# Optimization experiments

Measured on AMD Instinct MI355X. Metric: run time of the kernel, lower is better.

Reference implementation:

```python
import jax, jax.numpy as jnp
import numpy as np

B, N, C, H, F = 4, 256, 256, 8, 64  # batch, nodes, in_channels, heads, n_hidden


def setup_inputs() -> dict:
    key = jax.random.key(0)
    k1, k2, k3, k4, k5 = jax.random.split(key, 5)
    x = jax.random.normal(k1, (B, N, C), jnp.float32)
    W_l = jax.random.normal(k2, (C, H * F), jnp.float32) / np.sqrt(C)
    W_r = jax.random.normal(k3, (C, H * F), jnp.float32) / np.sqrt(C)
    attn_w = jax.random.normal(k4, (F,), jnp.float32) / np.sqrt(F)
    adj = jax.random.randint(k5, (N, N, H), 0, 2, jnp.int32)
    # guarantee at least one unmasked head per (i, j) pair so the
    # softmax-over-heads (dim=-1 in the source) never sees all -inf
    adj = adj.at[:, :, 0].set(1)
    return {"x": x, "W_l": W_l, "W_r": W_r, "attn_w": attn_w, "adj": adj}


def reference(x, W_l, W_r, attn_w, adj):
    b, n, _ = x.shape
    g_l = (x @ W_l).reshape(b, n, H, F)
    g_r = (x @ W_r).reshape(b, n, H, F)
    # torch: g_l.repeat(1,n,1,1) + g_r.repeat_interleave(n,dim=1), then
    # view(b,n,n,h,f)  =>  g_sum[b,i,j,h,f] = g_r[b,i] + g_l[b,j]
    g_sum = g_r[:, :, None] + g_l[:, None, :]          # [b,i,j,h,f]
    e = jnp.einsum('bijhf,f->bijh', jax.nn.leaky_relu(g_sum, 0.2), attn_w)
    e = jnp.where(adj == 0, -jnp.inf, e)               # adj broadcasts over batch
    a = jax.nn.softmax(e, axis=-1)                     # softmax over heads, per source (dim=-1)
    out = jnp.einsum('bijh,bjhf->bihf', a, g_r)        # aggregate over neighbors j
    return out.reshape(b, n, H * F)                    # is_concat=True
```

## Files before the change

### kernel.cpp

```cpp
#include <hip/hip_runtime.h>
#include <hip/hip_bf16.h>

typedef _Float16 h2 __attribute__((ext_vector_type(2)));

constexpr int kB = 4, kN = 256, kC = 256, kH = 8, kF = 64, kHF = 512;
constexpr int kIPB = 4;

union H2U { h2 h; unsigned int u; };

__global__ __launch_bounds__(256) void gat_gemm_kernel(
    const float* __restrict__ x,
    const float* __restrict__ Wl,
    const float* __restrict__ Wr,
    unsigned int* __restrict__ gl,
    unsigned int* __restrict__ gr)
{
    __shared__ float xs[4][kC];
    const int rowBase = blockIdx.x * 4;
    const float* Wm = (blockIdx.y == 0) ? Wl : Wr;
    unsigned int* gout = (blockIdx.y == 0) ? gl : gr;

    const int tid = threadIdx.x;

    {
        const int r = tid >> 6;
        const int kc = (tid & 63) * 4;
        *(float4*)&xs[r][kc] = *(const float4*)(x + (rowBase + r) * kC + kc);
    }
    __syncthreads();

    const int c0 = tid * 2;
    float acc[4][2];
#pragma unroll
    for (int r = 0; r < 4; ++r) { acc[r][0] = 0.f; acc[r][1] = 0.f; }

    for (int k = 0; k < kC; k += 4) {
        float2 wv[4];
#pragma unroll
        for (int kk = 0; kk < 4; ++kk)
            wv[kk] = *(const float2*)(Wm + (k + kk) * kHF + c0);
#pragma unroll
        for (int r = 0; r < 4; ++r) {
            float4 xv = *(const float4*)&xs[r][k];
            acc[r][0] = fmaf(xv.x, wv[0].x, acc[r][0]);
            acc[r][1] = fmaf(xv.x, wv[0].y, acc[r][1]);
            acc[r][0] = fmaf(xv.y, wv[1].x, acc[r][0]);
            acc[r][1] = fmaf(xv.y, wv[1].y, acc[r][1]);
            acc[r][0] = fmaf(xv.z, wv[2].x, acc[r][0]);
            acc[r][1] = fmaf(xv.z, wv[2].y, acc[r][1]);
            acc[r][0] = fmaf(xv.w, wv[3].x, acc[r][0]);
            acc[r][1] = fmaf(xv.w, wv[3].y, acc[r][1]);
        }
    }

#pragma unroll
    for (int r = 0; r < 4; ++r) {
        H2U p; p.h = (h2){(_Float16)acc[r][0], (_Float16)acc[r][1]};
        gout[((rowBase + r) * kHF + c0) >> 1] = p.u;
    }
}

__global__ __launch_bounds__(512) void gat_attn_kernel(
    const unsigned int* __restrict__ gl,
    const unsigned int* __restrict__ gr,
    const float* __restrict__ attn_w,
    const int* __restrict__ adj,
    float* __restrict__ out)
{
    __shared__ float red[8 * kIPB * kHF];

    const int bi0 = blockIdx.x * kIPB;
    const int b = bi0 >> 8;
    const int i0 = bi0 & 255;
    const int tid = threadIdx.x;
    const int wv = tid >> 6;
    const int lane = tid & 63;
    const int h = lane >> 3;
    const int fg = lane & 7;
    const int fbase = fg * 8;

    h2 gri[kIPB][4];
#pragma unroll
    for (int ii = 0; ii < kIPB; ++ii) {
        uint4 pk = *(const uint4*)(gr +
            (((size_t)(bi0 + ii) * kHF + h * kF + fbase) >> 1));
        H2U a0, a1, a2, a3;
        a0.u = pk.x; a1.u = pk.y; a2.u = pk.z; a3.u = pk.w;
        gri[ii][0] = a0.h; gri[ii][1] = a1.h; gri[ii][2] = a2.h; gri[ii][3] = a3.h;
    }
    h2 w2[4];
    {
        float4 wa = *(const float4*)(attn_w + fbase);
        float4 wb = *(const float4*)(attn_w + fbase + 4);
        w2[0] = (h2){(_Float16)wa.x, (_Float16)wa.y};
        w2[1] = (h2){(_Float16)wa.z, (_Float16)wa.w};
        w2[2] = (h2){(_Float16)wb.x, (_Float16)wb.y};
        w2[3] = (h2){(_Float16)wb.z, (_Float16)wb.w};
    }

    float acc[kIPB][8];
#pragma unroll
    for (int ii = 0; ii < kIPB; ++ii)
#pragma unroll
        for (int q = 0; q < 8; ++q) acc[ii][q] = 0.f;

    const h2 c02 = (h2){(_Float16)0.2f, (_Float16)0.2f};
    const size_t gcolbase = (size_t)(b * kN) * kHF + h * kF + fbase;
    const int adjbase = i0 * kN * kH + h;

    for (int j = wv; j < kN; j += 8) {
        const size_t off = (gcolbase + (size_t)j * kHF) >> 1;
        uint4 ga = *(const uint4*)(gl + off);
        uint4 gb = *(const uint4*)(gr + off);

        int am[kIPB];
#pragma unroll
        for (int ii = 0; ii < kIPB; ++ii)
            am[ii] = adj[adjbase + (ii * kN + j) * kH];

        h2 gl2[4], gr2[4];
        { H2U t; t.u = ga.x; gl2[0] = t.h; t.u = ga.y; gl2[1] = t.h;
                 t.u = ga.z; gl2[2] = t.h; t.u = ga.w; gl2[3] = t.h;
                 t.u = gb.x; gr2[0] = t.h; t.u = gb.y; gr2[1] = t.h;
                 t.u = gb.z; gr2[2] = t.h; t.u = gb.w; gr2[3] = t.h; }

        float grf[8];
#pragma unroll
        for (int q = 0; q < 4; ++q) {
            grf[2 * q]     = (float)gr2[q].x;
            grf[2 * q + 1] = (float)gr2[q].y;
        }

#pragma unroll
        for (int ii = 0; ii < kIPB; ++ii) {
            float e = 0.f;
#pragma unroll
            for (int q = 0; q < 4; ++q) {
                h2 s = gri[ii][q] + gl2[q];
                h2 u = __builtin_elementwise_max(s, c02 * s);
                e = __builtin_amdgcn_fdot2(u, w2[q], e, false);
            }
            e += __shfl_xor(e, 1);
            e += __shfl_xor(e, 2);
            e += __shfl_xor(e, 4);

            e = am[ii] ? e : -1e30f;

            float ex = __expf(e);
            float den = ex;
            den += __shfl_xor(den, 8);
            den += __shfl_xor(den, 16);
            den += __shfl_xor(den, 32);
            float a = ex * __builtin_amdgcn_rcpf(den);

#pragma unroll
            for (int q = 0; q < 8; ++q)
                acc[ii][q] = fmaf(a, grf[q], acc[ii][q]);
        }
    }

#pragma unroll
    for (int ii = 0; ii < kIPB; ++ii) {
        float* rp = &red[(wv * kIPB + ii) * kHF + lane * 8];
#pragma unroll
        for (int q = 0; q < 8; ++q) rp[q] = acc[ii][q];
    }
    __syncthreads();

#pragma unroll
    for (int ii = 0; ii < kIPB; ++ii) {
        float s = 0.f;
#pragma unroll
        for (int w8 = 0; w8 < 8; ++w8)
            s += red[(w8 * kIPB + ii) * kHF + tid];
        out[(size_t)(bi0 + ii) * kHF + tid] = s;
    }
}

extern "C" void kernel_launch(void* const* d_in, const int* in_sizes, int n_in,
                              void* d_out, int out_size, void* d_ws, size_t ws_size,
                              hipStream_t stream) {
    const float* x  = (const float*)d_in[0];
    const float* Wl = (const float*)d_in[1];
    const float* Wr = (const float*)d_in[2];
    const float* aw = (const float*)d_in[3];
    const int* adj  = (const int*)d_in[4];

    unsigned int* gl = (unsigned int*)d_ws;
    unsigned int* gr = gl + (size_t)kB * kN * kHF / 2;

    dim3 g1(kB * kN / 4, 2);
    gat_gemm_kernel<<<g1, 256, 0, stream>>>(x, Wl, Wr, gl, gr);

    gat_attn_kernel<<<kB * kN / kIPB, 512, 0, stream>>>(
        gl, gr, aw, adj, (float*)d_out);
}
```

Before: 113.0 us.

## Restructure attention kernel: one row per block, lane per (j,head), fp16 accumulation

The attention kernel is remapped so each block handles a single output row i. Each lane owns one (neighbor j, head) pair and computes the full 64-wide dot product itself, which removes the intra-head shuffle reduction. The adjacency row is packed into a byte mask in shared memory, and the weighted aggregation accumulates in packed fp16 before shuffle and shared-memory reductions. The GEMM kernel also gets software prefetching of the next W slice. The trade-offs are fp16 accumulation over 256 neighbors, which may lose precision, and higher register pressure from the 32-element arrays. The gr row that each block re-reads is no longer shared across 4 rows per block.

```diff
diff --git a/kernel.cpp b/kernel.cpp
--- a/kernel.cpp
+++ b/kernel.cpp
@@ -4,7 +4,6 @@
 typedef _Float16 h2 __attribute__((ext_vector_type(2)));
 
 constexpr int kB = 4, kN = 256, kC = 256, kH = 8, kF = 64, kHF = 512;
-constexpr int kIPB = 4;
 
 union H2U { h2 h; unsigned int u; };
 
@@ -34,11 +33,17 @@
 #pragma unroll
     for (int r = 0; r < 4; ++r) { acc[r][0] = 0.f; acc[r][1] = 0.f; }
 
+    float2 wv[4], wn[4];
+#pragma unroll
+    for (int kk = 0; kk < 4; ++kk)
+        wv[kk] = *(const float2*)(Wm + kk * kHF + c0);
+
     for (int k = 0; k < kC; k += 4) {
-        float2 wv[4];
-#pragma unroll
-        for (int kk = 0; kk < 4; ++kk)
-            wv[kk] = *(const float2*)(Wm + (k + kk) * kHF + c0);
+        if (k + 4 < kC) {
+#pragma unroll
+            for (int kk = 0; kk < 4; ++kk)
+                wn[kk] = *(const float2*)(Wm + (k + 4 + kk) * kHF + c0);
+        }
 #pragma unroll
         for (int r = 0; r < 4; ++r) {
             float4 xv = *(const float4*)&xs[r][k];
@@ -51,6 +56,8 @@
             acc[r][0] = fmaf(xv.w, wv[3].x, acc[r][0]);
             acc[r][1] = fmaf(xv.w, wv[3].y, acc[r][1]);
         }
+#pragma unroll
+        for (int kk = 0; kk < 4; ++kk) wv[kk] = wn[kk];
     }
 
 #pragma unroll
@@ -60,120 +67,145 @@
     }
 }
 
-__global__ __launch_bounds__(512) void gat_attn_kernel(
+__global__ __launch_bounds__(256, 4) void gat_attn_kernel(
     const unsigned int* __restrict__ gl,
     const unsigned int* __restrict__ gr,
     const float* __restrict__ attn_w,
     const int* __restrict__ adj,
     float* __restrict__ out)
 {
-    __shared__ float red[8 * kIPB * kHF];
-
-    const int bi0 = blockIdx.x * kIPB;
-    const int b = bi0 >> 8;
-    const int i0 = bi0 & 255;
+    __shared__ float red[4][kHF];
+    __shared__ unsigned char msk[kN];
+
+    const int bi = blockIdx.x;
+    const int b = bi >> 8;
+    const int i = bi & 255;
     const int tid = threadIdx.x;
     const int wv = tid >> 6;
     const int lane = tid & 63;
-    const int h = lane >> 3;
-    const int fg = lane & 7;
-    const int fbase = fg * 8;
-
-    h2 gri[kIPB][4];
-#pragma unroll
-    for (int ii = 0; ii < kIPB; ++ii) {
-        uint4 pk = *(const uint4*)(gr +
-            (((size_t)(bi0 + ii) * kHF + h * kF + fbase) >> 1));
-        H2U a0, a1, a2, a3;
-        a0.u = pk.x; a1.u = pk.y; a2.u = pk.z; a3.u = pk.w;
-        gri[ii][0] = a0.h; gri[ii][1] = a1.h; gri[ii][2] = a2.h; gri[ii][3] = a3.h;
-    }
-    h2 w2[4];
+    const int jl = lane >> 3;
+    const int h = lane & 7;
+
     {
-        float4 wa = *(const float4*)(attn_w + fbase);
-        float4 wb = *(const float4*)(attn_w + fbase + 4);
-        w2[0] = (h2){(_Float16)wa.x, (_Float16)wa.y};
-        w2[1] = (h2){(_Float16)wa.z, (_Float16)wa.w};
-        w2[2] = (h2){(_Float16)wb.x, (_Float16)wb.y};
-        w2[3] = (h2){(_Float16)wb.z, (_Float16)wb.w};
-    }
-
-    float acc[kIPB][8];
-#pragma unroll
-    for (int ii = 0; ii < kIPB; ++ii)
-#pragma unroll
-        for (int q = 0; q < 8; ++q) acc[ii][q] = 0.f;
+        const int* ap = adj + (i * kN + tid) * kH;
+        uint4 a0 = *(const uint4*)ap;
+        uint4 a1 = *(const uint4*)(ap + 4);
+        unsigned int m = 0;
+        m |= (a0.x != 0) << 0; m |= (a0.y != 0) << 1;
+        m |= (a0.z != 0) << 2; m |= (a0.w != 0) << 3;
+        m |= (a1.x != 0) << 4; m |= (a1.y != 0) << 5;
+        m |= (a1.z != 0) << 6; m |= (a1.w != 0) << 7;
+        msk[tid] = (unsigned char)m;
+    }
+
+    h2 gri[32];
+    {
+        const uint4* gp = (const uint4*)(gr + (bi * 256 + h * 32));
+#pragma unroll
+        for (int q = 0; q < 8; ++q) {
+            uint4 p = gp[q];
+            H2U t;
+            t.u = p.x; gri[q * 4 + 0] = t.h;
+            t.u = p.y; gri[q * 4 + 1] = t.h;
+            t.u = p.z; gri[q * 4 + 2] = t.h;
+            t.u = p.w; gri[q * 4 + 3] = t.h;
+        }
+    }
+
+    unsigned int wsg[32];
+#pragma unroll
+    for (int q = 0; q < 32; ++q) {
+        float2 wp = *(const float2*)(attn_w + q * 2);
+        H2U t; t.h = (h2){(_Float16)wp.x, (_Float16)wp.y};
+        wsg[q] = __builtin_amdgcn_readfirstlane(t.u);
+    }
+
+    h2 acc[32];
+#pragma unroll
+    for (int q = 0; q < 32; ++q) acc[q] = (h2){(_Float16)0.f, (_Float16)0.f};
 
     const h2 c02 = (h2){(_Float16)0.2f, (_Float16)0.2f};
-    const size_t gcolbase = (size_t)(b * kN) * kHF + h * kF + fbase;
-    const int adjbase = i0 * kN * kH + h;
-
-    for (int j = wv; j < kN; j += 8) {
-        const size_t off = (gcolbase + (size_t)j * kHF) >> 1;
-        uint4 ga = *(const uint4*)(gl + off);
-        uint4 gb = *(const uint4*)(gr + off);
-
-        int am[kIPB];
-#pragma unroll
-        for (int ii = 0; ii < kIPB; ++ii)
-            am[ii] = adj[adjbase + (ii * kN + j) * kH];
-
-        h2 gl2[4], gr2[4];
-        { H2U t; t.u = ga.x; gl2[0] = t.h; t.u = ga.y; gl2[1] = t.h;
-                 t.u = ga.z; gl2[2] = t.h; t.u = ga.w; gl2[3] = t.h;
-                 t.u = gb.x; gr2[0] = t.h; t.u = gb.y; gr2[1] = t.h;
-                 t.u = gb.z; gr2[2] = t.h; t.u = gb.w; gr2[3] = t.h; }
-
-        float grf[8];
-#pragma unroll
-        for (int q = 0; q < 4; ++q) {
-            grf[2 * q]     = (float)gr2[q].x;
-            grf[2 * q + 1] = (float)gr2[q].y;
-        }
-
-#pragma unroll
-        for (int ii = 0; ii < kIPB; ++ii) {
-            float e = 0.f;
-#pragma unroll
-            for (int q = 0; q < 4; ++q) {
-                h2 s = gri[ii][q] + gl2[q];
-                h2 u = __builtin_elementwise_max(s, c02 * s);
-                e = __builtin_amdgcn_fdot2(u, w2[q], e, false);
-            }
-            e += __shfl_xor(e, 1);
-            e += __shfl_xor(e, 2);
-            e += __shfl_xor(e, 4);
-
-            e = am[ii] ? e : -1e30f;
-
-            float ex = __expf(e);
-            float den = ex;
-            den += __shfl_xor(den, 8);
-            den += __shfl_xor(den, 16);
-            den += __shfl_xor(den, 32);
-            float a = ex * __builtin_amdgcn_rcpf(den);
-
-#pragma unroll
-            for (int q = 0; q < 8; ++q)
-                acc[ii][q] = fmaf(a, grf[q], acc[ii][q]);
-        }
-    }
-
-#pragma unroll
-    for (int ii = 0; ii < kIPB; ++ii) {
-        float* rp = &red[(wv * kIPB + ii) * kHF + lane * 8];
-#pragma unroll
-        for (int q = 0; q < 8; ++q) rp[q] = acc[ii][q];
-    }
+
     __syncthreads();
 
-#pragma unroll
-    for (int ii = 0; ii < kIPB; ++ii) {
-        float s = 0.f;
-#pragma unroll
-        for (int w8 = 0; w8 < 8; ++w8)
-            s += red[(w8 * kIPB + ii) * kHF + tid];
-        out[(size_t)(bi0 + ii) * kHF + tid] = s;
+    unsigned int goff = (unsigned int)(b * kN * 256) + (wv * 8 + jl) * 256 + h * 32;
+    int j = wv * 8 + jl;
+
+    for (int round = 0; round < 8; ++round) {
+        const uint4* gp = (const uint4*)(gl + goff);
+        uint4 P[8];
+#pragma unroll
+        for (int q = 0; q < 8; ++q) P[q] = gp[q];
+
+        float e = 0.f;
+#pragma unroll
+        for (int q = 0; q < 8; ++q) {
+            H2U t0, t1, t2, t3, w0, w1, w2u, w3;
+            t0.u = P[q].x; t1.u = P[q].y; t2.u = P[q].z; t3.u = P[q].w;
+            w0.u = wsg[q * 4 + 0]; w1.u = wsg[q * 4 + 1];
+            w2u.u = wsg[q * 4 + 2]; w3.u = wsg[q * 4 + 3];
+            h2 s0 = gri[q * 4 + 0] + t0.h;
+            h2 s1 = gri[q * 4 + 1] + t1.h;
+            h2 s2 = gri[q * 4 + 2] + t2.h;
+            h2 s3 = gri[q * 4 + 3] + t3.h;
+            h2 u0 = __builtin_elementwise_max(s0, c02 * s0);
+            h2 u1 = __builtin_elementwise_max(s1, c02 * s1);
+            h2 u2 = __builtin_elementwise_max(s2, c02 * s2);
+            h2 u3 = __builtin_elementwise_max(s3, c02 * s3);
+            e = __builtin_amdgcn_fdot2(u0, w0.h, e, false);
+            e = __builtin_amdgcn_fdot2(u1, w1.h, e, false);
+            e = __builtin_amdgcn_fdot2(u2, w2u.h, e, false);
+            e = __builtin_amdgcn_fdot2(u3, w3.h, e, false);
+        }
+
+        const unsigned int mbit = ((unsigned int)msk[j] >> h) & 1u;
+        e = mbit ? e : -1e30f;
+        float ex = __expf(e);
+        float den = ex;
+        den += __shfl_xor(den, 1);
+        den += __shfl_xor(den, 2);
+        den += __shfl_xor(den, 4);
+        float a = ex * __builtin_amdgcn_rcpf(den);
+        h2 a2 = (h2){(_Float16)a, (_Float16)a};
+
+        const uint4* gq = (const uint4*)(gr + goff);
+#pragma unroll
+        for (int q = 0; q < 8; ++q) {
+            uint4 p = gq[q];
+            H2U t0, t1, t2, t3;
+            t0.u = p.x; t1.u = p.y; t2.u = p.z; t3.u = p.w;
+            acc[q * 4 + 0] = __builtin_elementwise_fma(a2, t0.h, acc[q * 4 + 0]);
+            acc[q * 4 + 1] = __builtin_elementwise_fma(a2, t1.h, acc[q * 4 + 1]);
+            acc[q * 4 + 2] = __builtin_elementwise_fma(a2, t2.h, acc[q * 4 + 2]);
+            acc[q * 4 + 3] = __builtin_elementwise_fma(a2, t3.h, acc[q * 4 + 3]);
+        }
+
+        goff += 32 * 256;
+        j += 32;
+    }
+
+#pragma unroll
+    for (int q = 0; q < 32; ++q) {
+        H2U t; t.h = acc[q];
+        H2U r;
+        r.u = (unsigned int)__shfl_xor((int)t.u, 8);  t.h = t.h + r.h;
+        r.u = (unsigned int)__shfl_xor((int)t.u, 16); t.h = t.h + r.h;
+        r.u = (unsigned int)__shfl_xor((int)t.u, 32); t.h = t.h + r.h;
+        acc[q] = t.h;
+    }
+
+#pragma unroll
+    for (int k = 0; k < 4; ++k) {
+        h2 v = acc[jl * 4 + k];
+        float2 f = make_float2((float)v.x, (float)v.y);
+        *(float2*)&red[wv][h * 64 + jl * 8 + k * 2] = f;
+    }
+    __syncthreads();
+
+#pragma unroll
+    for (int c = tid; c < kHF; c += 256) {
+        float s = red[0][c] + red[1][c] + red[2][c] + red[3][c];
+        out[(size_t)bi * kHF + c] = s;
     }
 }
 
@@ -192,6 +224,6 @@
     dim3 g1(kB * kN / 4, 2);
     gat_gemm_kernel<<<g1, 256, 0, stream>>>(x, Wl, Wr, gl, gr);
 
-    gat_attn_kernel<<<kB * kN / kIPB, 512, 0, stream>>>(
+    gat_attn_kernel<<<kB * kN, 256, 0, stream>>>(
         gl, gr, aw, adj, (float*)d_out);
 }
```

Measured after the change: 191.6 us. 1.7x slower.
